# Kernel tuning notes

Hardware: AMD Instinct MI355X
Metric: run time of the kernel (lower is better)

Reference implementation:

```python
import jax, jax.numpy as jnp
import numpy as np

B, S, D, H = 2, 4096, 1024, 16
HD = D // H  # 64


def setup_inputs() -> dict:
    key = jax.random.key(0)
    ks = jax.random.split(key, 6)
    return {
        "x": jax.random.normal(ks[0], (B, S, D), dtype=jnp.float32),
        "mask": jax.random.normal(ks[1], (B, S, S), dtype=jnp.float32),
        "Wqkv": jax.random.normal(ks[2], (D, 3 * D), dtype=jnp.float32) * 0.02,
        "bqkv": jax.random.normal(ks[3], (3 * D,), dtype=jnp.float32) * 0.02,
        "Wo": jax.random.normal(ks[4], (D, D), dtype=jnp.float32) * 0.02,
        "bo": jax.random.normal(ks[5], (D,), dtype=jnp.float32) * 0.02,
    }


def reference(x, mask, Wqkv, bqkv, Wo, bo):
    b, s, d = x.shape
    # fused QKV projection: [B,S,3D]
    qkv = jnp.einsum('bsd,de->bse', x, Wqkv) + bqkv
    # [B,S,H,3*HD] -> [B,H,S,3*HD]
    qkv = qkv.reshape(b, s, H, 3 * HD).transpose(0, 2, 1, 3)
    q, k, v = jnp.split(qkv, 3, axis=-1)  # each [B,H,S,HD]
    scale = 1.0 / jnp.sqrt(jnp.asarray(HD, dtype=x.dtype))
    scores = jnp.einsum('bhqe,bhke->bhqk', q, k) * scale  # [B,H,S,S]
    scores = scores + mask[:, None, :, :]  # additive mask broadcast over heads
    attn = jax.nn.softmax(scores, axis=-1)
    values = jnp.einsum('bhqk,bhke->bhqe', attn, v)  # [B,H,S,HD]
    # NOTE: faithful to original TF code: reshape WITHOUT transposing heads back
    values = values.reshape(b, s, d)
    out = jnp.einsum('bsd,de->bse', values, Wo) + bo
    return out
```

## Files before the change

kernel.cpp:

```cpp
#include <hip/hip_runtime.h>
#include <hip/hip_bf16.h>

#define DEV __device__ __forceinline__

typedef unsigned short u16;
typedef __attribute__((ext_vector_type(4))) float f32x4;
typedef __attribute__((ext_vector_type(8))) short s16x8;

static constexpr int Bc = 2, Hc = 16, Sc = 4096, Dc = 1024, HDc = 64;

DEV u16 f2bf(float f) {
  unsigned x = __float_as_uint(f);
  x += 0x7FFFu + ((x >> 16) & 1u);
  return (u16)(x >> 16);
}
DEV float bf2f(u16 u) { return __uint_as_float(((unsigned)u) << 16); }

DEV unsigned cvtpk_bf16(float lo, float hi) {
  unsigned r;
  asm("v_cvt_pk_bf16_f32 %0, %1, %2" : "=v"(r) : "v"(lo), "v"(hi));
  return r;
}

DEV void gload_lds16(const void* g, void* l) {
  __builtin_amdgcn_global_load_lds((const __attribute__((address_space(1))) void*)g,
                                   (__attribute__((address_space(3))) void*)l, 16, 0, 0);
}

DEV f32x4 mfma16(s16x8 a, s16x8 b, f32x4 c) {
  return __builtin_amdgcn_mfma_f32_16x16x32_bf16(a, b, c, 0, 0, 0);
}

DEV f32x4 fzero4() { f32x4 v; v[0] = v[1] = v[2] = v[3] = 0.f; return v; }

__global__ void cvt_f32_bf16(const float* __restrict__ in, u16* __restrict__ out, size_t n) {
  size_t i = ((size_t)blockIdx.x * blockDim.x + threadIdx.x) * 4;
  size_t stride = (size_t)gridDim.x * blockDim.x * 4;
  for (; i < n; i += stride) {
    float4 v = *(const float4*)(in + i);
    u16 a = f2bf(v.x), b = f2bf(v.y), c = f2bf(v.z), d = f2bf(v.w);
    *(ushort4*)(out + i) = make_ushort4(a, b, c, d);
  }
}

__global__ void transpose_cvt(const float* __restrict__ in, u16* __restrict__ out, int R, int C) {
  __shared__ u16 t[64][72];
  int nct = C >> 6;
  int tr = blockIdx.x / nct, tc = blockIdx.x % nct;
  int r0 = tr << 6, c0 = tc << 6;
  int lr = threadIdx.x >> 2;
  int lc0 = (threadIdx.x & 3) << 4;
  const float* src = in + (size_t)(r0 + lr) * C + c0 + lc0;
#pragma unroll
  for (int j = 0; j < 16; j += 4) {
    float4 v = *(const float4*)(src + j);
    t[lr][lc0 + j + 0] = f2bf(v.x);
    t[lr][lc0 + j + 1] = f2bf(v.y);
    t[lr][lc0 + j + 2] = f2bf(v.z);
    t[lr][lc0 + j + 3] = f2bf(v.w);
  }
  __syncthreads();
  u16* dst = out + (size_t)(c0 + lr) * R + r0 + lc0;
#pragma unroll
  for (int j = 0; j < 16; j += 4) {
    u16 a = t[lc0 + j + 0][lr], b = t[lc0 + j + 1][lr], c = t[lc0 + j + 2][lr], d = t[lc0 + j + 3][lr];
    *(ushort4*)(dst + j) = make_ushort4(a, b, c, d);
  }
}

template <int MODE>
__global__ __launch_bounds__(256, 2) void gemm128(
    const u16* __restrict__ A, const u16* __restrict__ BT, const float* __restrict__ bias,
    void* __restrict__ out0, u16* __restrict__ out1, u16* __restrict__ out2,
    int N, int K, int grid_n) {
  __shared__ u16 Al[128 * 64];
  __shared__ u16 Bl[128 * 64];
  int bid = blockIdx.x;
  int bn = bid % grid_n, bm = bid / grid_n;
  int m0 = bm * 128, n0 = bn * 128;
  int tid = threadIdx.x, lane = tid & 63, wid = tid >> 6;
  int wm = wid >> 1, wn = wid & 1;
  int fr = lane & 15, fg = lane >> 4;

  f32x4 acc[4][4];
#pragma unroll
  for (int mi = 0; mi < 4; ++mi)
#pragma unroll
    for (int ni = 0; ni < 4; ++ni) acc[mi][ni] = fzero4();

  for (int kt = 0; kt < K; kt += 64) {
    const u16* Ag = A + (size_t)m0 * K + kt;
    const u16* Bg = BT + (size_t)n0 * K + kt;
#pragma unroll
    for (int it = 0; it < 4; ++it) {
      int L = it * 4096 + wid * 1024 + lane * 16;
      int row = L >> 7;
      int sch = ((L >> 4) & 7) ^ (row & 7);
      gload_lds16(Ag + (size_t)row * K + sch * 8, (char*)Al + it * 4096 + wid * 1024);
      gload_lds16(Bg + (size_t)row * K + sch * 8, (char*)Bl + it * 4096 + wid * 1024);
    }
    __syncthreads();
#pragma unroll
    for (int c = 0; c < 2; ++c) {
      s16x8 af[4], bfr[4];
#pragma unroll
      for (int mi = 0; mi < 4; ++mi) {
        int row = wm * 64 + mi * 16 + fr;
        int ch = (c * 4 + fg) ^ (row & 7);
        af[mi] = *(const s16x8*)((const char*)Al + row * 128 + ch * 16);
      }
#pragma unroll
      for (int ni = 0; ni < 4; ++ni) {
        int row = wn * 64 + ni * 16 + fr;
        int ch = (c * 4 + fg) ^ (row & 7);
        bfr[ni] = *(const s16x8*)((const char*)Bl + row * 128 + ch * 16);
      }
#pragma unroll
      for (int mi = 0; mi < 4; ++mi)
#pragma unroll
        for (int ni = 0; ni < 4; ++ni) acc[mi][ni] = mfma16(af[mi], bfr[ni], acc[mi][ni]);
    }
    __syncthreads();
  }

  if constexpr (MODE == 0) {
    u16* qb = (u16*)out0;
    u16* kb = out1;
    u16* vT = out2;
#pragma unroll
    for (int ni = 0; ni < 4; ++ni) {
      int n = n0 + wn * 64 + ni * 16 + fr;
      float bv = bias[n];
      int h = n / 192;
      int c = n % 192;
      int part = c >> 6;
      int e = c & 63;
#pragma unroll
      for (int mi = 0; mi < 4; ++mi) {
        int m = m0 + wm * 64 + mi * 16 + fg * 4;
        int b = m >> 12;
        int s = m & 4095;
        size_t bh = (size_t)b * Hc + h;
        if (part == 2) {
          u16 a0 = f2bf(acc[mi][ni][0] + bv), a1 = f2bf(acc[mi][ni][1] + bv);
          u16 a2 = f2bf(acc[mi][ni][2] + bv), a3 = f2bf(acc[mi][ni][3] + bv);
          *(ushort4*)(vT + ((bh * HDc + e) * (size_t)Sc + s)) = make_ushort4(a0, a1, a2, a3);
        } else {
          u16* dst = (part == 0 ? qb : kb) + ((bh * Sc + s) * (size_t)HDc + e);
#pragma unroll
          for (int r = 0; r < 4; ++r) dst[(size_t)r * HDc] = f2bf(acc[mi][ni][r] + bv);
        }
      }
    }
  } else {
    float* O = (float*)out0;
#pragma unroll
    for (int ni = 0; ni < 4; ++ni) {
      int n = n0 + wn * 64 + ni * 16 + fr;
      float bv = bias[n];
#pragma unroll
      for (int mi = 0; mi < 4; ++mi) {
        int m = m0 + wm * 64 + mi * 16 + fg * 4;
#pragma unroll
        for (int r = 0; r < 4; ++r) O[(size_t)(m + r) * N + n] = acc[mi][ni][r] + bv;
      }
    }
  }
}

__global__ __launch_bounds__(256, 6) void attn_kernel(
    const u16* __restrict__ qb, const u16* __restrict__ kb, const u16* __restrict__ vT,
    const float* __restrict__ maskp, u16* __restrict__ vals) {
  __shared__ u16 Kl[64 * 64];
  __shared__ u16 Vl[64 * 64];
  __shared__ char Pl[4 * 16 * 144];

  int bid = ((blockIdx.x & 7) << 8) | (blockIdx.x >> 3);
  int h = bid & 15, b = (bid >> 4) & 1, qt = bid >> 5;
  int tid = threadIdx.x;
  int lane = tid & 63, wid = tid >> 6;
  int fr = lane & 15, fg = lane >> 4;
  size_t bh = (size_t)b * Hc + h;
  int q0 = qt * 64;
  int q = q0 + wid * 16 + fr;

  const u16* Qrow = qb + ((bh * Sc) + q) * (size_t)HDc;
  s16x8 qa0 = *(const s16x8*)(Qrow + fg * 8);
  s16x8 qa1 = *(const s16x8*)(Qrow + 32 + fg * 8);

  f32x4 o[4];
#pragma unroll
  for (int ef = 0; ef < 4; ++ef) o[ef] = fzero4();
  float mrun = -1e30f, lrun = 0.f;

  const u16* Kg = kb + bh * (size_t)Sc * HDc;
  const u16* Vg = vT + bh * (size_t)HDc * Sc;
  char* pw = (char*)Pl + wid * 2304 + fr * 144;
  const float SCALE = 0.125f;
  const float LOG2E = 1.44269504088896340736f;

  int e8 = tid & 7;
  int r5 = tid >> 3;
  int rr = r5 & 7;
  int swc = (e8 ^ rr) << 4;
  int ldsw0 = (0 * 32 + r5) * 128 + swc;
  int ldsw1 = (1 * 32 + r5) * 128 + swc;
  const u16* KgL0 = Kg + (size_t)(0 * 32 + r5) * HDc + e8 * 8;
  const u16* KgL1 = Kg + (size_t)(1 * 32 + r5) * HDc + e8 * 8;
  const u16* VgL0 = Vg + (size_t)(0 * 32 + r5) * Sc + e8 * 8;
  const u16* VgL1 = Vg + (size_t)(1 * 32 + r5) * Sc + e8 * 8;

  int kroff0 = fr * 128 + ((fg ^ (fr & 7)) << 4);
  int kroff1 = fr * 128 + (((4 + fg) ^ (fr & 7)) << 4);

  const float* mk = maskp + ((size_t)b * Sc + q) * Sc;

  {
    uint4 k0 = *(const uint4*)(KgL0);
    uint4 k1 = *(const uint4*)(KgL1);
    uint4 v0 = *(const uint4*)(VgL0);
    uint4 v1 = *(const uint4*)(VgL1);
    *(uint4*)((char*)Kl + ldsw0) = k0;
    *(uint4*)((char*)Kl + ldsw1) = k1;
    *(uint4*)((char*)Vl + ldsw0) = v0;
    *(uint4*)((char*)Vl + ldsw1) = v1;
  }
  __syncthreads();

  for (int kt = 0; kt < Sc / 64; ++kt) {
    int ktn = (kt < Sc / 64 - 1) ? kt + 1 : kt;
    uint4 kn0 = *(const uint4*)(KgL0 + (size_t)ktn * 4096);
    uint4 kn1 = *(const uint4*)(KgL1 + (size_t)ktn * 4096);
    uint4 vn0 = *(const uint4*)(VgL0 + (size_t)ktn * 64);
    uint4 vn1 = *(const uint4*)(VgL1 + (size_t)ktn * 64);

    const float* mrow = mk + kt * 64 + fg * 4;
    float4 mf0 = *(const float4*)(mrow);
    float4 mf1 = *(const float4*)(mrow + 16);
    float4 mf2 = *(const float4*)(mrow + 32);
    float4 mf3 = *(const float4*)(mrow + 48);

    f32x4 sa[4];
#pragma unroll
    for (int f = 0; f < 4; ++f) sa[f] = fzero4();
    __builtin_amdgcn_s_setprio(1);
#pragma unroll
    for (int f = 0; f < 4; ++f) {
      s16x8 kf = *(const s16x8*)((const char*)Kl + f * 2048 + kroff0);
      sa[f] = mfma16(kf, qa0, sa[f]);
    }
#pragma unroll
    for (int f = 0; f < 4; ++f) {
      s16x8 kf = *(const s16x8*)((const char*)Kl + f * 2048 + kroff1);
      sa[f] = mfma16(kf, qa1, sa[f]);
    }
    __builtin_amdgcn_s_setprio(0);

    float t[4][4];
#pragma unroll
    for (int r = 0; r < 4; ++r) {
      t[0][r] = fmaf(sa[0][r], SCALE, (&mf0.x)[r]);
      t[1][r] = fmaf(sa[1][r], SCALE, (&mf1.x)[r]);
      t[2][r] = fmaf(sa[2][r], SCALE, (&mf2.x)[r]);
      t[3][r] = fmaf(sa[3][r], SCALE, (&mf3.x)[r]);
    }

    float x0 = fmaxf(fmaxf(t[0][0], t[0][1]), t[0][2]);
    float x1 = fmaxf(fmaxf(t[0][3], t[1][0]), t[1][1]);
    float x2 = fmaxf(fmaxf(t[1][2], t[1][3]), t[2][0]);
    float x3 = fmaxf(fmaxf(t[2][1], t[2][2]), t[2][3]);
    float x4 = fmaxf(fmaxf(t[3][0], t[3][1]), t[3][2]);
    float mt = fmaxf(fmaxf(fmaxf(x0, x1), x2), fmaxf(fmaxf(x3, x4), t[3][3]));
    mt = fmaxf(mt, __shfl_xor(mt, 16, 64));
    mt = fmaxf(mt, __shfl_xor(mt, 32, 64));

    if (!__all(mt <= mrun + 8.0f)) {
      float mnew = fmaxf(mrun, mt);
      float al = __builtin_amdgcn_exp2f((mrun - mnew) * LOG2E);
      mrun = mnew;
      lrun *= al;
#pragma unroll
      for (int ef = 0; ef < 4; ++ef) o[ef] *= al;
    }

    float nm = -mrun * LOG2E;
    float p[4][4];
    float ss0 = 0.f, ss1 = 0.f;
#pragma unroll
    for (int f = 0; f < 4; ++f) {
      float p0 = __builtin_amdgcn_exp2f(fmaf(t[f][0], LOG2E, nm));
      float p1 = __builtin_amdgcn_exp2f(fmaf(t[f][1], LOG2E, nm));
      float p2 = __builtin_amdgcn_exp2f(fmaf(t[f][2], LOG2E, nm));
      float p3 = __builtin_amdgcn_exp2f(fmaf(t[f][3], LOG2E, nm));
      p[f][0] = p0; p[f][1] = p1; p[f][2] = p2; p[f][3] = p3;
      ss0 += (p0 + p1);
      ss1 += (p2 + p3);
    }
    float ssum = ss0 + ss1;
    ssum += __shfl_xor(ssum, 16, 64);
    ssum += __shfl_xor(ssum, 32, 64);
    lrun += ssum;

#pragma unroll
    for (int f = 0; f < 4; ++f) {
      uint2 pk;
      pk.x = cvtpk_bf16(p[f][0], p[f][1]);
      pk.y = cvtpk_bf16(p[f][2], p[f][3]);
      *(uint2*)(pw + f * 32 + fg * 8) = pk;
    }

    s16x8 pa0 = *(const s16x8*)(pw + fg * 16);
    s16x8 pa1 = *(const s16x8*)(pw + 64 + fg * 16);
    __builtin_amdgcn_s_setprio(1);
#pragma unroll
    for (int ef = 0; ef < 4; ++ef) {
      s16x8 vf = *(const s16x8*)((const char*)Vl + ef * 2048 + kroff0);
      o[ef] = mfma16(vf, pa0, o[ef]);
    }
#pragma unroll
    for (int ef = 0; ef < 4; ++ef) {
      s16x8 vf = *(const s16x8*)((const char*)Vl + ef * 2048 + kroff1);
      o[ef] = mfma16(vf, pa1, o[ef]);
    }
    __builtin_amdgcn_s_setprio(0);

    __syncthreads();
    *(uint4*)((char*)Kl + ldsw0) = kn0;
    *(uint4*)((char*)Kl + ldsw1) = kn1;
    *(uint4*)((char*)Vl + ldsw0) = vn0;
    *(uint4*)((char*)Vl + ldsw1) = vn1;
    __syncthreads();
  }

  float inv = 1.f / lrun;
  u16* vbase = vals + (size_t)b * Sc * Dc + (size_t)h * Sc * HDc + (size_t)q * HDc;
#pragma unroll
  for (int ef = 0; ef < 4; ++ef) {
    ushort4 ov = make_ushort4(f2bf(o[ef][0] * inv), f2bf(o[ef][1] * inv),
                              f2bf(o[ef][2] * inv), f2bf(o[ef][3] * inv));
    *(ushort4*)(vbase + ef * 16 + fg * 4) = ov;
  }
}

extern "C" void kernel_launch(void* const* d_in, const int* in_sizes, int n_in,
                              void* d_out, int out_size, void* d_ws, size_t ws_size,
                              hipStream_t stream) {
  (void)in_sizes; (void)n_in; (void)out_size; (void)ws_size;
  const float* x    = (const float*)d_in[0];
  const float* mask = (const float*)d_in[1];
  const float* Wqkv = (const float*)d_in[2];
  const float* bqkv = (const float*)d_in[3];
  const float* Wo   = (const float*)d_in[4];
  const float* bo   = (const float*)d_in[5];
  float* out = (float*)d_out;
  char* ws = (char*)d_ws;

  u16* xb    = (u16*)(ws + 0);
  u16* wqkvT = (u16*)(ws + 16777216);
  u16* woT   = (u16*)(ws + 23068672);
  u16* qb    = (u16*)(ws + 25165824);
  u16* kb    = (u16*)(ws + 41943040);
  u16* vT    = (u16*)(ws + 58720256);
  u16* vals  = (u16*)(ws + 75497472);

  cvt_f32_bf16<<<dim3(2048), dim3(256), 0, stream>>>(x, xb, (size_t)8388608);
  transpose_cvt<<<dim3(768), dim3(256), 0, stream>>>(Wqkv, wqkvT, 1024, 3072);
  transpose_cvt<<<dim3(256), dim3(256), 0, stream>>>(Wo, woT, 1024, 1024);

  gemm128<0><<<dim3(1536), dim3(256), 0, stream>>>(xb, wqkvT, bqkv, (void*)qb, kb, vT,
                                                   3072, 1024, 24);
  attn_kernel<<<dim3(2048), dim3(256), 0, stream>>>(qb, kb, vT, mask, vals);
  gemm128<1><<<dim3(512), dim3(256), 0, stream>>>(vals, woT, bo, (void*)out, nullptr, nullptr,
                                                  1024, 1024, 8);
}
```

Baseline: 489.2 us.

## Precast mask to bf16, use direct-to-LDS K/V loads, widen attention blocks

Result: no change. 497.5 us (+1.7%).

```diff
diff --git a/kernel.cpp b/kernel.cpp
--- a/kernel.cpp
+++ b/kernel.cpp
@@ -168,20 +168,21 @@
   }
 }
 
-__global__ __launch_bounds__(256, 6) void attn_kernel(
+template <int MB>
+__global__ __launch_bounds__(512, 6) void attn_kernel(
     const u16* __restrict__ qb, const u16* __restrict__ kb, const u16* __restrict__ vT,
-    const float* __restrict__ maskp, u16* __restrict__ vals) {
+    const void* __restrict__ maskp, u16* __restrict__ vals) {
   __shared__ u16 Kl[64 * 64];
   __shared__ u16 Vl[64 * 64];
-  __shared__ char Pl[4 * 16 * 144];
-
-  int bid = ((blockIdx.x & 7) << 8) | (blockIdx.x >> 3);
+  __shared__ char Pl[8 * 16 * 144];
+
+  int bid = ((blockIdx.x & 7) << 7) | (blockIdx.x >> 3);
   int h = bid & 15, b = (bid >> 4) & 1, qt = bid >> 5;
   int tid = threadIdx.x;
   int lane = tid & 63, wid = tid >> 6;
   int fr = lane & 15, fg = lane >> 4;
   size_t bh = (size_t)b * Hc + h;
-  int q0 = qt * 64;
+  int q0 = qt * 128;
   int q = q0 + wid * 16 + fr;
 
   const u16* Qrow = qb + ((bh * Sc) + q) * (size_t)HDc;
@@ -199,46 +200,33 @@
   const float SCALE = 0.125f;
   const float LOG2E = 1.44269504088896340736f;
 
-  int e8 = tid & 7;
-  int r5 = tid >> 3;
-  int rr = r5 & 7;
-  int swc = (e8 ^ rr) << 4;
-  int ldsw0 = (0 * 32 + r5) * 128 + swc;
-  int ldsw1 = (1 * 32 + r5) * 128 + swc;
-  const u16* KgL0 = Kg + (size_t)(0 * 32 + r5) * HDc + e8 * 8;
-  const u16* KgL1 = Kg + (size_t)(1 * 32 + r5) * HDc + e8 * 8;
-  const u16* VgL0 = Vg + (size_t)(0 * 32 + r5) * Sc + e8 * 8;
-  const u16* VgL1 = Vg + (size_t)(1 * 32 + r5) * Sc + e8 * 8;
+  int srow = wid * 8 + (lane >> 3);
+  int sch = (lane & 7) ^ (srow & 7);
+  const u16* KgS = Kg + (size_t)srow * HDc + sch * 8;
+  const u16* VgS = Vg + (size_t)srow * Sc + sch * 8;
+  char* KlD = (char*)Kl + wid * 1024;
+  char* VlD = (char*)Vl + wid * 1024;
 
   int kroff0 = fr * 128 + ((fg ^ (fr & 7)) << 4);
   int kroff1 = fr * 128 + (((4 + fg) ^ (fr & 7)) << 4);
 
-  const float* mk = maskp + ((size_t)b * Sc + q) * Sc;
-
-  {
-    uint4 k0 = *(const uint4*)(KgL0);
-    uint4 k1 = *(const uint4*)(KgL1);
-    uint4 v0 = *(const uint4*)(VgL0);
-    uint4 v1 = *(const uint4*)(VgL1);
-    *(uint4*)((char*)Kl + ldsw0) = k0;
-    *(uint4*)((char*)Kl + ldsw1) = k1;
-    *(uint4*)((char*)Vl + ldsw0) = v0;
-    *(uint4*)((char*)Vl + ldsw1) = v1;
-  }
-  __syncthreads();
+  const u16* mk_b = (const u16*)maskp + ((size_t)b * Sc + q) * Sc + fg * 4;
+  const float* mk_f = (const float*)maskp + ((size_t)b * Sc + q) * Sc + fg * 4;
 
   for (int kt = 0; kt < Sc / 64; ++kt) {
-    int ktn = (kt < Sc / 64 - 1) ? kt + 1 : kt;
-    uint4 kn0 = *(const uint4*)(KgL0 + (size_t)ktn * 4096);
-    uint4 kn1 = *(const uint4*)(KgL1 + (size_t)ktn * 4096);
-    uint4 vn0 = *(const uint4*)(VgL0 + (size_t)ktn * 64);
-    uint4 vn1 = *(const uint4*)(VgL1 + (size_t)ktn * 64);
-
-    const float* mrow = mk + kt * 64 + fg * 4;
-    float4 mf0 = *(const float4*)(mrow);
-    float4 mf1 = *(const float4*)(mrow + 16);
-    float4 mf2 = *(const float4*)(mrow + 32);
-    float4 mf3 = *(const float4*)(mrow + 48);
+    gload_lds16(KgS + (size_t)kt * 4096, KlD);
+    gload_lds16(VgS + (size_t)kt * 64, VlD);
+
+    ushort4 m4[4];
+    float4 mf[4];
+    if (MB) {
+#pragma unroll
+      for (int f = 0; f < 4; ++f) m4[f] = *(const ushort4*)(mk_b + kt * 64 + f * 16);
+    } else {
+#pragma unroll
+      for (int f = 0; f < 4; ++f) mf[f] = *(const float4*)(mk_f + kt * 64 + f * 16);
+    }
+    __syncthreads();
 
     f32x4 sa[4];
 #pragma unroll
@@ -258,11 +246,18 @@
 
     float t[4][4];
 #pragma unroll
-    for (int r = 0; r < 4; ++r) {
-      t[0][r] = fmaf(sa[0][r], SCALE, (&mf0.x)[r]);
-      t[1][r] = fmaf(sa[1][r], SCALE, (&mf1.x)[r]);
-      t[2][r] = fmaf(sa[2][r], SCALE, (&mf2.x)[r]);
-      t[3][r] = fmaf(sa[3][r], SCALE, (&mf3.x)[r]);
+    for (int f = 0; f < 4; ++f) {
+      if (MB) {
+        t[f][0] = fmaf(sa[f][0], SCALE, bf2f(m4[f].x));
+        t[f][1] = fmaf(sa[f][1], SCALE, bf2f(m4[f].y));
+        t[f][2] = fmaf(sa[f][2], SCALE, bf2f(m4[f].z));
+        t[f][3] = fmaf(sa[f][3], SCALE, bf2f(m4[f].w));
+      } else {
+        t[f][0] = fmaf(sa[f][0], SCALE, mf[f].x);
+        t[f][1] = fmaf(sa[f][1], SCALE, mf[f].y);
+        t[f][2] = fmaf(sa[f][2], SCALE, mf[f].z);
+        t[f][3] = fmaf(sa[f][3], SCALE, mf[f].w);
+      }
     }
 
     float x0 = fmaxf(fmaxf(t[0][0], t[0][1]), t[0][2]);
@@ -325,11 +320,6 @@
     __builtin_amdgcn_s_setprio(0);
 
     __syncthreads();
-    *(uint4*)((char*)Kl + ldsw0) = kn0;
-    *(uint4*)((char*)Kl + ldsw1) = kn1;
-    *(uint4*)((char*)Vl + ldsw0) = vn0;
-    *(uint4*)((char*)Vl + ldsw1) = vn1;
-    __syncthreads();
   }
 
   float inv = 1.f / lrun;
@@ -345,7 +335,7 @@
 extern "C" void kernel_launch(void* const* d_in, const int* in_sizes, int n_in,
                               void* d_out, int out_size, void* d_ws, size_t ws_size,
                               hipStream_t stream) {
-  (void)in_sizes; (void)n_in; (void)out_size; (void)ws_size;
+  (void)in_sizes; (void)n_in; (void)out_size;
   const float* x    = (const float*)d_in[0];
   const float* mask = (const float*)d_in[1];
   const float* Wqkv = (const float*)d_in[2];
@@ -362,14 +352,21 @@
   u16* kb    = (u16*)(ws + 41943040);
   u16* vT    = (u16*)(ws + 58720256);
   u16* vals  = (u16*)(ws + 75497472);
+  u16* maskb = (u16*)(ws + 92274688);
+  int use_mb = (ws_size >= 159383552ull) ? 1 : 0;
 
   cvt_f32_bf16<<<dim3(2048), dim3(256), 0, stream>>>(x, xb, (size_t)8388608);
+  if (use_mb)
+    cvt_f32_bf16<<<dim3(4096), dim3(256), 0, stream>>>(mask, maskb, (size_t)33554432);
   transpose_cvt<<<dim3(768), dim3(256), 0, stream>>>(Wqkv, wqkvT, 1024, 3072);
   transpose_cvt<<<dim3(256), dim3(256), 0, stream>>>(Wo, woT, 1024, 1024);
 
   gemm128<0><<<dim3(1536), dim3(256), 0, stream>>>(xb, wqkvT, bqkv, (void*)qb, kb, vT,
                                                    3072, 1024, 24);
-  attn_kernel<<<dim3(2048), dim3(256), 0, stream>>>(qb, kb, vT, mask, vals);
+  if (use_mb)
+    attn_kernel<1><<<dim3(1024), dim3(512), 0, stream>>>(qb, kb, vT, (const void*)maskb, vals);
+  else
+    attn_kernel<0><<<dim3(1024), dim3(512), 0, stream>>>(qb, kb, vT, (const void*)mask, vals);
   gemm128<1><<<dim3(512), dim3(256), 0, stream>>>(vals, woT, bo, (void*)out, nullptr, nullptr,
                                                   1024, 1024, 8);
 }
```
